# Kernel optimization log

Hardware: AMD Instinct MI355X
Metric: run time of the kernel (lower is better)

## Reference

```python
import jax, jax.numpy as jnp
import numpy as np

N_NODES = 50000
N_EDGES = 800000
D_IN = 64
D_OUT = 64
D_HID = 64
EPS = 1e-5


def _init_params(key):
    ks = jax.random.split(key, 12)
    s = 0.05
    p = {}
    p["W_lin"] = jax.random.normal(ks[0], (D_IN, D_OUT), jnp.float32) * s
    p["W_src"] = jax.random.normal(ks[1], (D_IN, D_OUT), jnp.float32) * s
    p["W_dst"] = jax.random.normal(ks[2], (D_IN, D_OUT), jnp.float32) * s
    p["pos_w1"] = jax.random.normal(ks[3], (3, D_HID), jnp.float32) * s
    p["pos_b1"] = jnp.zeros((D_HID,), jnp.float32)
    p["pos_w2"] = jax.random.normal(ks[4], (D_HID, D_OUT), jnp.float32) * s
    p["pos_b2"] = jnp.zeros((D_OUT,), jnp.float32)
    p["attn_w1"] = jax.random.normal(ks[5], (D_OUT, D_HID), jnp.float32) * s
    p["attn_b1"] = jnp.zeros((D_HID,), jnp.float32)
    p["attn_w2"] = jax.random.normal(ks[6], (D_HID, D_OUT), jnp.float32) * s
    p["attn_b2"] = jnp.zeros((D_OUT,), jnp.float32)
    p["gamma"] = jnp.ones((D_OUT,), jnp.float32)
    p["beta"] = jnp.zeros((D_OUT,), jnp.float32)
    return p


def setup_inputs() -> dict:
    key = jax.random.key(0)
    k1, k2, k3, k4 = jax.random.split(key, 4)
    inp = {
        "x": jax.random.normal(k1, (N_NODES, D_IN), jnp.float32),
        "pos": jax.random.normal(k2, (N_NODES, 3), jnp.float32),
        "edge_index": jax.random.randint(k3, (2, N_EDGES), 0, N_NODES, jnp.int64),
    }
    inp.update(_init_params(k4))
    return inp


def _segment_softmax(alpha, seg, num_segments):
    # channel-wise softmax over edges sharing the same destination node
    m = jax.ops.segment_max(alpha, seg, num_segments=num_segments)  # [N, D]
    e = jnp.exp(alpha - m[seg])
    z = jax.ops.segment_sum(e, seg, num_segments=num_segments)  # [N, D]
    return e / (z[seg] + 1e-16)


def reference(x, pos, edge_index, W_lin, W_src, W_dst,
              pos_w1, pos_b1, pos_w2, pos_b2,
              attn_w1, attn_b1, attn_w2, attn_b2, gamma, beta):
    N = x.shape[0]
    # add self loops (PointTransformerConv default add_self_loops=True)
    loops = jnp.arange(N, dtype=edge_index.dtype)
    src = jnp.concatenate([edge_index[0], loops])  # j
    dst = jnp.concatenate([edge_index[1], loops])  # i (aggregation target)

    x_val = x @ W_lin          # [N, D] value projection
    a_src = x @ W_src          # alpha_j source term
    a_dst = x @ W_dst          # alpha_i destination term

    # per-edge positional encoding: pos_nn(pos_i - pos_j), two Linears, no activation
    rel = pos[dst] - pos[src]                         # [E, 3]
    delta = (rel @ pos_w1 + pos_b1) @ pos_w2 + pos_b2  # [E, D]

    # attention logits: attn_nn(alpha_i - alpha_j + delta)
    alpha = a_dst[dst] - a_src[src] + delta
    alpha = (alpha @ attn_w1 + attn_b1) @ attn_w2 + attn_b2  # [E, D]
    alpha = _segment_softmax(alpha, dst, N)

    # message and scatter-sum aggregation
    msg = alpha * (x_val[src] + delta)                # [E, D]
    out = jax.ops.segment_sum(msg, dst, num_segments=N)  # [N, D]

    out = jax.nn.elu(out)

    # BatchNorm over nodes (training-mode batch stats, biased var, eps=1e-5)
    mean = jnp.mean(out, axis=0)
    var = jnp.var(out, axis=0)
    out = (out - mean) * jax.lax.rsqrt(var + EPS) * gamma + beta
    return out
```

## Files before the change

### kernel.cpp

```cpp
#include <hip/hip_runtime.h>
#include <cmath>


__device__ __forceinline__ unsigned bf16r(float f) {
    unsigned u = __float_as_uint(f);
    return (u + 0x7fffu + ((u >> 16) & 1u)) >> 16;
}
__device__ __forceinline__ float bfhi(unsigned u) { return __uint_as_float(u & 0xffff0000u); }
__device__ __forceinline__ float bflo(unsigned u) { return __uint_as_float(u << 16); }

__device__ __forceinline__ void gemm_tile(const float (*xs)[68], const float (*Wl)[64],
                                          int tx, int ty, float acc[4][4])
{
    #pragma unroll
    for (int i = 0; i < 4; ++i)
        #pragma unroll
        for (int j = 0; j < 4; ++j) acc[i][j] = 0.f;
    for (int k = 0; k < 64; k += 4) {
        float4 b0 = *(const float4*)&Wl[k + 0][4 * tx];
        float4 b1 = *(const float4*)&Wl[k + 1][4 * tx];
        float4 b2 = *(const float4*)&Wl[k + 2][4 * tx];
        float4 b3 = *(const float4*)&Wl[k + 3][4 * tx];
        #pragma unroll
        for (int i = 0; i < 4; ++i) {
            float4 a = *(const float4*)&xs[4 * ty + i][k];
            acc[i][0] += a.x * b0.x + a.y * b1.x + a.z * b2.x + a.w * b3.x;
            acc[i][1] += a.x * b0.y + a.y * b1.y + a.z * b2.y + a.w * b3.y;
            acc[i][2] += a.x * b0.z + a.y * b1.z + a.z * b2.z + a.w * b3.z;
            acc[i][3] += a.x * b0.w + a.y * b1.w + a.z * b2.w + a.w * b3.w;
        }
    }
}

__global__ __launch_bounds__(256) void k_pre1(
    const float* __restrict__ attn_w1, const float* __restrict__ attn_w2,
    const float* __restrict__ pos_w1, const float* __restrict__ pos_b1,
    const float* __restrict__ pos_w2, const float* __restrict__ pos_b2,
    float* __restrict__ A2, float* __restrict__ M3, float* __restrict__ bc,
    int* __restrict__ cnt, float* __restrict__ stats, int n_nodes)
{
    int t = threadIdx.x;
    if (blockIdx.x == 0) {
        __shared__ __align__(16) float As[64][68];
        __shared__ __align__(16) float Bs[64][64];
        int lk = t & 63, lr = t >> 6;
        for (int i = 0; i < 16; ++i) {
            As[lr + 4 * i][lk] = attn_w1[(lr + 4 * i) * 64 + lk];
            Bs[lr + 4 * i][lk] = attn_w2[(lr + 4 * i) * 64 + lk];
        }
        __syncthreads();
        int tx = t & 15, ty = t >> 4;
        float acc[4][4];
        gemm_tile(As, Bs, tx, ty, acc);
        #pragma unroll
        for (int i = 0; i < 4; ++i)
            *(float4*)&A2[(4 * ty + i) * 64 + 4 * tx] =
                make_float4(acc[i][0], acc[i][1], acc[i][2], acc[i][3]);
    } else if (blockIdx.x == 1) {
        int c = t & 63, q = t >> 6;
        if (q < 3) {
            float acc = 0.f;
            for (int h = 0; h < 64; ++h) acc += pos_w1[q * 64 + h] * pos_w2[h * 64 + c];
            M3[q * 64 + c] = acc;
        } else {
            float accb = 0.f;
            for (int h = 0; h < 64; ++h) accb += pos_b1[h] * pos_w2[h * 64 + c];
            bc[c] = accb + pos_b2[c];
        }
    } else {
        if (blockIdx.x == 2 && t < 128) stats[t] = 0.f;
        int idx = (blockIdx.x - 2) * 256 + t;
        int stride = (gridDim.x - 2) * 256;
        for (int i = idx; i < n_nodes; i += stride) cnt[i] = 0;
    }
}

__global__ __launch_bounds__(256) void k_pre2(
    const float* __restrict__ W_src, const float* __restrict__ A2,
    const float* __restrict__ M3,
    float* __restrict__ Wsrc2, float* __restrict__ M5)
{
    int t = threadIdx.x;
    if (blockIdx.x == 0) {
        __shared__ __align__(16) float As[64][68];
        __shared__ __align__(16) float Bs[64][64];
        int lk = t & 63, lr = t >> 6;
        for (int i = 0; i < 16; ++i) {
            As[lr + 4 * i][lk] = W_src[(lr + 4 * i) * 64 + lk];
            Bs[lr + 4 * i][lk] = A2[(lr + 4 * i) * 64 + lk];
        }
        __syncthreads();
        int tx = t & 15, ty = t >> 4;
        float acc[4][4];
        gemm_tile(As, Bs, tx, ty, acc);
        #pragma unroll
        for (int i = 0; i < 4; ++i)
            *(float4*)&Wsrc2[(4 * ty + i) * 64 + 4 * tx] =
                make_float4(acc[i][0], acc[i][1], acc[i][2], acc[i][3]);
    } else {
        int c = t & 63, q = t >> 6;
        if (q < 3) {
            float acc = 0.f;
            for (int k = 0; k < 64; ++k) acc += M3[q * 64 + k] * A2[k * 64 + c];
            M5[q * 64 + c] = acc;
        }
    }
}

__global__ __launch_bounds__(256, 4) void k_gemm_pair_hist(
    const float* __restrict__ x, const float* __restrict__ pos,
    const float* __restrict__ Wsrc2, const float* __restrict__ Wlin,
    const float* __restrict__ M3, const float* __restrict__ M5,
    unsigned* __restrict__ pairbf, int n_nodes,
    const int* __restrict__ ei, int* __restrict__ cnt, int n_edges, int G)
{
    int t = threadIdx.x;
    if ((int)blockIdx.x >= G) {
        int idx = ((int)blockIdx.x - G) * 256 + t;
        int stride = ((int)gridDim.x - G) * 256;
        for (int i = idx; i < n_edges; i += stride)
            atomicAdd(&cnt[ei[n_edges + i]], 1);
        return;
    }
    __shared__ __align__(16) float xs[64][68];
    __shared__ __align__(16) float Wl[64][64];
    __shared__ float ps[192];
    __shared__ float m3s[192], m5s[192];
    int tx = t & 15;
    int ty = t >> 4;
    int nbase = blockIdx.x * 64;
    int lk = t & 63;
    int lr = t >> 6;

    for (int i = 0; i < 16; ++i) {
        int n = lr + 4 * i;
        int gn = nbase + n;
        xs[n][lk] = (gn < n_nodes) ? x[gn * 64 + lk] : 0.f;
    }
    if (t < 192) {
        int gi = nbase * 3 + t;
        ps[t] = (gi < n_nodes * 3) ? pos[gi] : 0.f;
        m3s[t] = M3[t];
        m5s[t] = M5[t];
    }
    for (int i = 0; i < 16; ++i) Wl[lr + 4 * i][lk] = Wsrc2[(lr + 4 * i) * 64 + lk];
    __syncthreads();

    float acc_s[4][4];
    gemm_tile(xs, Wl, tx, ty, acc_s);

    __syncthreads();
    for (int i = 0; i < 16; ++i) Wl[lr + 4 * i][lk] = Wlin[(lr + 4 * i) * 64 + lk];
    __syncthreads();

    float acc_x[4][4];
    gemm_tile(xs, Wl, tx, ty, acc_x);

    #pragma unroll
    for (int i = 0; i < 4; ++i) {
        int n = 4 * ty + i;
        int gn = nbase + n;
        if (gn < n_nodes) {
            float px = ps[3 * n], py = ps[3 * n + 1], pz = ps[3 * n + 2];
            int c0 = 4 * tx;
            float g50 = px * m5s[c0]     + py * m5s[64 + c0]     + pz * m5s[128 + c0];
            float g51 = px * m5s[c0 + 1] + py * m5s[64 + c0 + 1] + pz * m5s[128 + c0 + 1];
            float g52 = px * m5s[c0 + 2] + py * m5s[64 + c0 + 2] + pz * m5s[128 + c0 + 2];
            float g53 = px * m5s[c0 + 3] + py * m5s[64 + c0 + 3] + pz * m5s[128 + c0 + 3];
            float g30 = px * m3s[c0]     + py * m3s[64 + c0]     + pz * m3s[128 + c0];
            float g31 = px * m3s[c0 + 1] + py * m3s[64 + c0 + 1] + pz * m3s[128 + c0 + 1];
            float g32 = px * m3s[c0 + 2] + py * m3s[64 + c0 + 2] + pz * m3s[128 + c0 + 2];
            float g33 = px * m3s[c0 + 3] + py * m3s[64 + c0 + 3] + pz * m3s[128 + c0 + 3];
            uint4 w;
            w.x = (bf16r(__expf(-(acc_s[i][0] + g50))) << 16) | bf16r(acc_x[i][0] - g30);
            w.y = (bf16r(__expf(-(acc_s[i][1] + g51))) << 16) | bf16r(acc_x[i][1] - g31);
            w.z = (bf16r(__expf(-(acc_s[i][2] + g52))) << 16) | bf16r(acc_x[i][2] - g32);
            w.w = (bf16r(__expf(-(acc_s[i][3] + g53))) << 16) | bf16r(acc_x[i][3] - g33);
            *(uint4*)&pairbf[gn * 64 + c0] = w;
        }
    }
}

#define SCAN_CHUNK 4096

__global__ __launch_bounds__(256) void k_scan_partial(const int* __restrict__ cnt,
                                                      int* __restrict__ bsum, int n)
{
    __shared__ int wsh[4];
    int b = blockIdx.x, t = threadIdx.x;
    int base = b * SCAN_CHUNK + t * 16;
    int s = 0;
    #pragma unroll
    for (int i = 0; i < 16; ++i) {
        int idx = base + i;
        if (idx < n) s += cnt[idx];
    }
    for (int off = 32; off; off >>= 1) s += __shfl_down(s, off, 64);
    int lane = t & 63, wv = t >> 6;
    if (lane == 0) wsh[wv] = s;
    __syncthreads();
    if (t == 0) bsum[b] = wsh[0] + wsh[1] + wsh[2] + wsh[3];
}

__global__ __launch_bounds__(256) void k_scan_final(const int* __restrict__ cnt,
                                                    const int* __restrict__ bsum,
                                                    int* __restrict__ rowptr,
                                                    int* __restrict__ cursor,
                                                    int n, int nch, int n_edges)
{
    __shared__ int wsh[4];
    __shared__ int bb;
    int b = blockIdx.x, t = threadIdx.x;
    if (t == 0) {
        int acc = 0;
        for (int c = 0; c < b; ++c) acc += bsum[c];
        bb = acc;
        if (b == nch - 1) rowptr[n] = n_edges;
    }
    int base = b * SCAN_CHUNK + t * 16;
    int v[16];
    int s = 0;
    #pragma unroll
    for (int i = 0; i < 16; ++i) {
        int idx = base + i;
        v[i] = (idx < n) ? cnt[idx] : 0;
        s += v[i];
    }
    int lane = t & 63, wv = t >> 6;
    int inc = s;
    for (int off = 1; off < 64; off <<= 1) {
        int u = __shfl_up(inc, off, 64);
        if (lane >= off) inc += u;
    }
    if (lane == 63) wsh[wv] = inc;
    __syncthreads();
    if (t == 0) {
        int acc = 0;
        for (int w = 0; w < 4; ++w) { int tmp = wsh[w]; wsh[w] = acc; acc += tmp; }
    }
    __syncthreads();
    int run = bb + wsh[wv] + inc - s;
    #pragma unroll
    for (int i = 0; i < 16; ++i) {
        int idx = base + i;
        if (idx < n) {
            rowptr[idx] = run;
            cursor[idx] = run;
            run += v[i];
        }
    }
}

__global__ __launch_bounds__(256) void k_scatter(const int* __restrict__ ei,
                                                 int* __restrict__ cursor,
                                                 int* __restrict__ csr_src,
                                                 int n_edges)
{
    int i = blockIdx.x * blockDim.x + threadIdx.x;
    if (i < n_edges) {
        int dst = ei[n_edges + i];
        int p = atomicAdd(&cursor[dst], 1);
        csr_src[p] = ei[i] * 64;
    }
}

__global__ __launch_bounds__(256) void k_gather(
    const int* __restrict__ rowptr, const int* __restrict__ csr_src,
    const unsigned* __restrict__ pairbf, const float* __restrict__ pos,
    const float* __restrict__ M3, const float* __restrict__ bc,
    float* __restrict__ out, float* __restrict__ stats, int n_nodes)
{
    int t = threadIdx.x;
    int c = t & 63;
    float bcc = bc[c];
    float m30 = M3[c], m31 = M3[64 + c], m32 = M3[128 + c];

    int wid = (blockIdx.x * blockDim.x + t) >> 6;
    int nw = (gridDim.x * blockDim.x) >> 6;

    float lsum = 0.f, lsq = 0.f;

    for (int i = wid; i < n_nodes; i += nw) {
        int beg = rowptr[i], end = rowptr[i + 1];
        float px = pos[3 * i], py = pos[3 * i + 1], pz = pos[3 * i + 2];
        float ddi = bcc + px * m30 + py * m31 + pz * m32;
        unsigned up = pairbf[i * 64 + c];
        float w = bfhi(up);
        float zz = w;
        float SS = w * bflo(up);

        int k = beg;
        for (; k + 8 <= end; k += 8) {
            int s0 = csr_src[k],     s1 = csr_src[k + 1];
            int s2 = csr_src[k + 2], s3 = csr_src[k + 3];
            int s4 = csr_src[k + 4], s5 = csr_src[k + 5];
            int s6 = csr_src[k + 6], s7 = csr_src[k + 7];
            unsigned u0 = pairbf[s0 + c], u1 = pairbf[s1 + c];
            unsigned u2 = pairbf[s2 + c], u3 = pairbf[s3 + c];
            unsigned u4 = pairbf[s4 + c], u5 = pairbf[s5 + c];
            unsigned u6 = pairbf[s6 + c], u7 = pairbf[s7 + c];
            float w0 = bfhi(u0), w1 = bfhi(u1), w2 = bfhi(u2), w3 = bfhi(u3);
            float w4 = bfhi(u4), w5 = bfhi(u5), w6 = bfhi(u6), w7 = bfhi(u7);
            zz += ((w0 + w1) + (w2 + w3)) + ((w4 + w5) + (w6 + w7));
            SS += w0 * bflo(u0) + w1 * bflo(u1) + w2 * bflo(u2) + w3 * bflo(u3)
                + w4 * bflo(u4) + w5 * bflo(u5) + w6 * bflo(u6) + w7 * bflo(u7);
        }
        for (; k < end; ++k) {
            unsigned u0 = pairbf[csr_src[k] + c];
            float w0 = bfhi(u0);
            zz += w0;
            SS += w0 * bflo(u0);
        }

        float v = SS / zz + ddi;
        v = (v > 0.f) ? v : expm1f(v);
        out[i * 64 + c] = v;
        lsum += v;
        lsq += v * v;
    }

    __shared__ float sred[256], sred2[256];
    sred[t] = lsum;
    sred2[t] = lsq;
    __syncthreads();
    if (t < 64) {
        float s = sred[t] + sred[t + 64] + sred[t + 128] + sred[t + 192];
        float q = sred2[t] + sred2[t + 64] + sred2[t + 128] + sred2[t + 192];
        unsafeAtomicAdd(&stats[t], s);
        unsafeAtomicAdd(&stats[64 + t], q);
    }
}

__global__ __launch_bounds__(256) void k_bn(
    float4* __restrict__ out4, const float* __restrict__ stats,
    const float* __restrict__ gamma, const float* __restrict__ beta,
    int total4, float inv_n)
{
    __shared__ float ssc[64], ssh[64];
    int t = threadIdx.x;
    if (t < 64) {
        float mean = stats[t] * inv_n;
        float var = stats[64 + t] * inv_n - mean * mean;
        float scale = (1.0f / sqrtf(var + 1e-5f)) * gamma[t];
        ssc[t] = scale;
        ssh[t] = beta[t] - mean * scale;
    }
    __syncthreads();
    for (int idx = blockIdx.x * blockDim.x + t; idx < total4;
         idx += gridDim.x * blockDim.x) {
        float4 v = out4[idx];
        int c0 = (idx << 2) & 63;
        v.x = v.x * ssc[c0]     + ssh[c0];
        v.y = v.y * ssc[c0 + 1] + ssh[c0 + 1];
        v.z = v.z * ssc[c0 + 2] + ssh[c0 + 2];
        v.w = v.w * ssc[c0 + 3] + ssh[c0 + 3];
        out4[idx] = v;
    }
}

extern "C" void kernel_launch(void* const* d_in, const int* in_sizes, int n_in,
                              void* d_out, int out_size, void* d_ws, size_t ws_size,
                              hipStream_t stream)
{
    const float* x        = (const float*)d_in[0];
    const float* pos      = (const float*)d_in[1];
    const int*   ei       = (const int*)d_in[2];
    const float* W_lin    = (const float*)d_in[3];
    const float* W_src    = (const float*)d_in[4];
    const float* pos_w1   = (const float*)d_in[6];
    const float* pos_b1   = (const float*)d_in[7];
    const float* pos_w2   = (const float*)d_in[8];
    const float* pos_b2   = (const float*)d_in[9];
    const float* attn_w1  = (const float*)d_in[10];
    const float* attn_w2  = (const float*)d_in[12];
    const float* gamma    = (const float*)d_in[14];
    const float* beta     = (const float*)d_in[15];

    int n_nodes = in_sizes[0] / 64;
    int n_edges = in_sizes[2] / 2;
    int total = n_nodes * 64;
    int nch = (n_nodes + SCAN_CHUNK - 1) / SCAN_CHUNK;

    unsigned* pairbf = (unsigned*)d_ws;
    float* A2    = (float*)(pairbf + total);
    float* Wsrc2 = A2 + 4096;
    float* M3    = Wsrc2 + 4096;
    float* M5    = M3 + 192;
    float* bc    = M5 + 192;
    float* stats = bc + 64;
    int*   cnt     = (int*)(stats + 128);
    int*   rowptr  = cnt + n_nodes;
    int*   cursor  = rowptr + n_nodes + 1;
    int*   csr_src = cursor + n_nodes;
    int*   bsum    = csr_src + n_edges;

    int G = (n_nodes + 63) / 64;

    k_pre1<<<18, 256, 0, stream>>>(attn_w1, attn_w2, pos_w1, pos_b1, pos_w2,
                                   pos_b2, A2, M3, bc, cnt, stats, n_nodes);
    k_pre2<<<2, 256, 0, stream>>>(W_src, A2, M3, Wsrc2, M5);
    k_gemm_pair_hist<<<G + 512, 256, 0, stream>>>(
        x, pos, Wsrc2, W_lin, M3, M5, pairbf, n_nodes, ei, cnt, n_edges, G);
    k_scan_partial<<<nch, 256, 0, stream>>>(cnt, bsum, n_nodes);
    k_scan_final<<<nch, 256, 0, stream>>>(cnt, bsum, rowptr, cursor,
                                          n_nodes, nch, n_edges);
    k_scatter<<<(n_edges + 255) / 256, 256, 0, stream>>>(ei, cursor, csr_src, n_edges);
    k_gather<<<2048, 256, 0, stream>>>(rowptr, csr_src, pairbf, pos, M3, bc,
                                       (float*)d_out, stats, n_nodes);
    k_bn<<<2048, 256, 0, stream>>>((float4*)d_out, stats, gamma, beta, total / 4,
                                   1.0f / (float)n_nodes);
}
```

Before: 203.6 us.

## Merge precompute kernels, vectorize histogram/scatter, split gather edges across half-waves

Folds the two small precompute kernels into one, computing Wsrc2 through shared memory and M5 through a chained small matmul, which removes a launch. The histogram and scatter kernels now read edge indices as int4, so each thread handles four edges. The gather kernel has each lane load two channels (uint2), and the two 32-lane halves of a wave take alternate 8-edge chunks, combined with a cross-half shuffle. The aim is more edges in flight per wave and fewer load instructions, at the cost of extra shuffles, half the lanes idling in the epilogue, and an alignment assumption for the int4 reads.

```diff
diff --git a/kernel.cpp b/kernel.cpp
--- a/kernel.cpp
+++ b/kernel.cpp
@@ -32,11 +32,13 @@
     }
 }
 
-__global__ __launch_bounds__(256) void k_pre1(
-    const float* __restrict__ attn_w1, const float* __restrict__ attn_w2,
+__global__ __launch_bounds__(256) void k_pre(
+    const float* __restrict__ W_src,
     const float* __restrict__ pos_w1, const float* __restrict__ pos_b1,
     const float* __restrict__ pos_w2, const float* __restrict__ pos_b2,
-    float* __restrict__ A2, float* __restrict__ M3, float* __restrict__ bc,
+    const float* __restrict__ attn_w1, const float* __restrict__ attn_w2,
+    float* __restrict__ Wsrc2, float* __restrict__ M3, float* __restrict__ M5,
+    float* __restrict__ bc,
     int* __restrict__ cnt, float* __restrict__ stats, int n_nodes)
 {
     int t = threadIdx.x;
@@ -52,58 +54,51 @@
         int tx = t & 15, ty = t >> 4;
         float acc[4][4];
         gemm_tile(As, Bs, tx, ty, acc);
+        __syncthreads();
         #pragma unroll
         for (int i = 0; i < 4; ++i)
-            *(float4*)&A2[(4 * ty + i) * 64 + 4 * tx] =
-                make_float4(acc[i][0], acc[i][1], acc[i][2], acc[i][3]);
+            #pragma unroll
+            for (int j = 0; j < 4; ++j)
+                Bs[4 * ty + i][4 * tx + j] = acc[i][j];
+        for (int i = 0; i < 16; ++i)
+            As[lr + 4 * i][lk] = W_src[(lr + 4 * i) * 64 + lk];
+        __syncthreads();
+        float acc2[4][4];
+        gemm_tile(As, Bs, tx, ty, acc2);
+        #pragma unroll
+        for (int i = 0; i < 4; ++i)
+            *(float4*)&Wsrc2[(4 * ty + i) * 64 + 4 * tx] =
+                make_float4(acc2[i][0], acc2[i][1], acc2[i][2], acc2[i][3]);
     } else if (blockIdx.x == 1) {
+        __shared__ float m3s[192], ts[192];
         int c = t & 63, q = t >> 6;
         if (q < 3) {
             float acc = 0.f;
             for (int h = 0; h < 64; ++h) acc += pos_w1[q * 64 + h] * pos_w2[h * 64 + c];
+            m3s[q * 64 + c] = acc;
             M3[q * 64 + c] = acc;
         } else {
             float accb = 0.f;
             for (int h = 0; h < 64; ++h) accb += pos_b1[h] * pos_w2[h * 64 + c];
             bc[c] = accb + pos_b2[c];
         }
+        __syncthreads();
+        if (q < 3) {
+            float acc = 0.f;
+            for (int k = 0; k < 64; ++k) acc += m3s[q * 64 + k] * attn_w1[k * 64 + c];
+            ts[q * 64 + c] = acc;
+        }
+        __syncthreads();
+        if (q < 3) {
+            float acc = 0.f;
+            for (int k = 0; k < 64; ++k) acc += ts[q * 64 + k] * attn_w2[k * 64 + c];
+            M5[q * 64 + c] = acc;
+        }
     } else {
         if (blockIdx.x == 2 && t < 128) stats[t] = 0.f;
         int idx = (blockIdx.x - 2) * 256 + t;
         int stride = (gridDim.x - 2) * 256;
         for (int i = idx; i < n_nodes; i += stride) cnt[i] = 0;
-    }
-}
-
-__global__ __launch_bounds__(256) void k_pre2(
-    const float* __restrict__ W_src, const float* __restrict__ A2,
-    const float* __restrict__ M3,
-    float* __restrict__ Wsrc2, float* __restrict__ M5)
-{
-    int t = threadIdx.x;
-    if (blockIdx.x == 0) {
-        __shared__ __align__(16) float As[64][68];
-        __shared__ __align__(16) float Bs[64][64];
-        int lk = t & 63, lr = t >> 6;
-        for (int i = 0; i < 16; ++i) {
-            As[lr + 4 * i][lk] = W_src[(lr + 4 * i) * 64 + lk];
-            Bs[lr + 4 * i][lk] = A2[(lr + 4 * i) * 64 + lk];
-        }
-        __syncthreads();
-        int tx = t & 15, ty = t >> 4;
-        float acc[4][4];
-        gemm_tile(As, Bs, tx, ty, acc);
-        #pragma unroll
-        for (int i = 0; i < 4; ++i)
-            *(float4*)&Wsrc2[(4 * ty + i) * 64 + 4 * tx] =
-                make_float4(acc[i][0], acc[i][1], acc[i][2], acc[i][3]);
-    } else {
-        int c = t & 63, q = t >> 6;
-        if (q < 3) {
-            float acc = 0.f;
-            for (int k = 0; k < 64; ++k) acc += M3[q * 64 + k] * A2[k * 64 + c];
-            M5[q * 64 + c] = acc;
-        }
     }
 }
 
@@ -118,7 +113,16 @@
     if ((int)blockIdx.x >= G) {
         int idx = ((int)blockIdx.x - G) * 256 + t;
         int stride = ((int)gridDim.x - G) * 256;
-        for (int i = idx; i < n_edges; i += stride)
+        int n4 = n_edges >> 2;
+        const int4* d4 = (const int4*)(ei + n_edges);
+        for (int i = idx; i < n4; i += stride) {
+            int4 d = d4[i];
+            atomicAdd(&cnt[d.x], 1);
+            atomicAdd(&cnt[d.y], 1);
+            atomicAdd(&cnt[d.z], 1);
+            atomicAdd(&cnt[d.w], 1);
+        }
+        for (int i = (n4 << 2) + idx; i < n_edges; i += stride)
             atomicAdd(&cnt[ei[n_edges + i]], 1);
         return;
     }
@@ -256,78 +260,116 @@
                                                  int* __restrict__ csr_src,
                                                  int n_edges)
 {
-    int i = blockIdx.x * blockDim.x + threadIdx.x;
-    if (i < n_edges) {
-        int dst = ei[n_edges + i];
-        int p = atomicAdd(&cursor[dst], 1);
-        csr_src[p] = ei[i] * 64;
+    int i4 = blockIdx.x * blockDim.x + threadIdx.x;
+    int n4 = n_edges >> 2;
+    if (i4 < n4) {
+        int4 sv = ((const int4*)ei)[i4];
+        int4 dv = ((const int4*)(ei + n_edges))[i4];
+        int p;
+        p = atomicAdd(&cursor[dv.x], 1); csr_src[p] = sv.x * 32;
+        p = atomicAdd(&cursor[dv.y], 1); csr_src[p] = sv.y * 32;
+        p = atomicAdd(&cursor[dv.z], 1); csr_src[p] = sv.z * 32;
+        p = atomicAdd(&cursor[dv.w], 1); csr_src[p] = sv.w * 32;
+    } else {
+        int e = (n4 << 2) + (i4 - n4);
+        if (e < n_edges) {
+            int dst = ei[n_edges + e];
+            int p = atomicAdd(&cursor[dst], 1);
+            csr_src[p] = ei[e] * 32;
+        }
     }
 }
 
 __global__ __launch_bounds__(256) void k_gather(
     const int* __restrict__ rowptr, const int* __restrict__ csr_src,
-    const unsigned* __restrict__ pairbf, const float* __restrict__ pos,
+    const uint2* __restrict__ pb2, const float* __restrict__ pos,
     const float* __restrict__ M3, const float* __restrict__ bc,
     float* __restrict__ out, float* __restrict__ stats, int n_nodes)
 {
     int t = threadIdx.x;
-    int c = t & 63;
-    float bcc = bc[c];
-    float m30 = M3[c], m31 = M3[64 + c], m32 = M3[128 + c];
+    int lane = t & 63;
+    int s = lane & 31;
+    int h = lane >> 5;
+    int c0 = 2 * s;
+    float bc0 = bc[c0], bc1 = bc[c0 + 1];
+    float m30a = M3[c0],     m31a = M3[64 + c0],     m32a = M3[128 + c0];
+    float m30b = M3[c0 + 1], m31b = M3[64 + c0 + 1], m32b = M3[128 + c0 + 1];
 
     int wid = (blockIdx.x * blockDim.x + t) >> 6;
     int nw = (gridDim.x * blockDim.x) >> 6;
 
-    float lsum = 0.f, lsq = 0.f;
+    float lsx = 0.f, lqx = 0.f, lsy = 0.f, lqy = 0.f;
 
     for (int i = wid; i < n_nodes; i += nw) {
         int beg = rowptr[i], end = rowptr[i + 1];
-        float px = pos[3 * i], py = pos[3 * i + 1], pz = pos[3 * i + 2];
-        float ddi = bcc + px * m30 + py * m31 + pz * m32;
-        unsigned up = pairbf[i * 64 + c];
-        float w = bfhi(up);
-        float zz = w;
-        float SS = w * bflo(up);
-
-        int k = beg;
-        for (; k + 8 <= end; k += 8) {
-            int s0 = csr_src[k],     s1 = csr_src[k + 1];
-            int s2 = csr_src[k + 2], s3 = csr_src[k + 3];
-            int s4 = csr_src[k + 4], s5 = csr_src[k + 5];
-            int s6 = csr_src[k + 6], s7 = csr_src[k + 7];
-            unsigned u0 = pairbf[s0 + c], u1 = pairbf[s1 + c];
-            unsigned u2 = pairbf[s2 + c], u3 = pairbf[s3 + c];
-            unsigned u4 = pairbf[s4 + c], u5 = pairbf[s5 + c];
-            unsigned u6 = pairbf[s6 + c], u7 = pairbf[s7 + c];
-            float w0 = bfhi(u0), w1 = bfhi(u1), w2 = bfhi(u2), w3 = bfhi(u3);
-            float w4 = bfhi(u4), w5 = bfhi(u5), w6 = bfhi(u6), w7 = bfhi(u7);
-            zz += ((w0 + w1) + (w2 + w3)) + ((w4 + w5) + (w6 + w7));
-            SS += w0 * bflo(u0) + w1 * bflo(u1) + w2 * bflo(u2) + w3 * bflo(u3)
-                + w4 * bflo(u4) + w5 * bflo(u5) + w6 * bflo(u6) + w7 * bflo(u7);
-        }
-        for (; k < end; ++k) {
-            unsigned u0 = pairbf[csr_src[k] + c];
-            float w0 = bfhi(u0);
-            zz += w0;
-            SS += w0 * bflo(u0);
-        }
-
-        float v = SS / zz + ddi;
-        v = (v > 0.f) ? v : expm1f(v);
-        out[i * 64 + c] = v;
-        lsum += v;
-        lsq += v * v;
-    }
-
-    __shared__ float sred[256], sred2[256];
-    sred[t] = lsum;
-    sred2[t] = lsq;
-    __syncthreads();
-    if (t < 64) {
-        float s = sred[t] + sred[t + 64] + sred[t + 128] + sred[t + 192];
-        float q = sred2[t] + sred2[t + 64] + sred2[t + 128] + sred2[t + 192];
-        unsafeAtomicAdd(&stats[t], s);
-        unsafeAtomicAdd(&stats[64 + t], q);
+        float zzx = 0.f, zzy = 0.f, SSx = 0.f, SSy = 0.f;
+        if (h == 0) {
+            uint2 up = pb2[i * 32 + s];
+            float w0 = bfhi(up.x), w1 = bfhi(up.y);
+            zzx = w0; SSx = w0 * bflo(up.x);
+            zzy = w1; SSy = w1 * bflo(up.y);
+        }
+        int k0 = beg;
+        for (; k0 + 16 <= end; k0 += 16) {
+            int kk = k0 + h * 8;
+            int e0 = csr_src[kk],     e1 = csr_src[kk + 1];
+            int e2 = csr_src[kk + 2], e3 = csr_src[kk + 3];
+            int e4 = csr_src[kk + 4], e5 = csr_src[kk + 5];
+            int e6 = csr_src[kk + 6], e7 = csr_src[kk + 7];
+            uint2 u0 = pb2[e0 + s], u1 = pb2[e1 + s];
+            uint2 u2 = pb2[e2 + s], u3 = pb2[e3 + s];
+            uint2 u4 = pb2[e4 + s], u5 = pb2[e5 + s];
+            uint2 u6 = pb2[e6 + s], u7 = pb2[e7 + s];
+            float a0 = bfhi(u0.x), a1 = bfhi(u1.x), a2 = bfhi(u2.x), a3 = bfhi(u3.x);
+            float a4 = bfhi(u4.x), a5 = bfhi(u5.x), a6 = bfhi(u6.x), a7 = bfhi(u7.x);
+            float b0 = bfhi(u0.y), b1 = bfhi(u1.y), b2 = bfhi(u2.y), b3 = bfhi(u3.y);
+            float b4 = bfhi(u4.y), b5 = bfhi(u5.y), b6 = bfhi(u6.y), b7 = bfhi(u7.y);
+            zzx += ((a0 + a1) + (a2 + a3)) + ((a4 + a5) + (a6 + a7));
+            zzy += ((b0 + b1) + (b2 + b3)) + ((b4 + b5) + (b6 + b7));
+            SSx += a0 * bflo(u0.x) + a1 * bflo(u1.x) + a2 * bflo(u2.x) + a3 * bflo(u3.x)
+                 + a4 * bflo(u4.x) + a5 * bflo(u5.x) + a6 * bflo(u6.x) + a7 * bflo(u7.x);
+            SSy += b0 * bflo(u0.y) + b1 * bflo(u1.y) + b2 * bflo(u2.y) + b3 * bflo(u3.y)
+                 + b4 * bflo(u4.y) + b5 * bflo(u5.y) + b6 * bflo(u6.y) + b7 * bflo(u7.y);
+        }
+        int r = end - k0;
+        int lo = h * 8;
+        int hi = min(r, 8 + lo);
+        for (int k = k0 + lo; k < k0 + hi; ++k) {
+            uint2 u = pb2[csr_src[k] + s];
+            float w0 = bfhi(u.x), w1 = bfhi(u.y);
+            zzx += w0; SSx += w0 * bflo(u.x);
+            zzy += w1; SSy += w1 * bflo(u.y);
+        }
+        zzx += __shfl_xor(zzx, 32, 64);
+        SSx += __shfl_xor(SSx, 32, 64);
+        zzy += __shfl_xor(zzy, 32, 64);
+        SSy += __shfl_xor(SSy, 32, 64);
+        if (h == 0) {
+            float px = pos[3 * i], py = pos[3 * i + 1], pz = pos[3 * i + 2];
+            float ddi0 = bc0 + px * m30a + py * m31a + pz * m32a;
+            float ddi1 = bc1 + px * m30b + py * m31b + pz * m32b;
+            float v0 = SSx / zzx + ddi0;
+            float v1 = SSy / zzy + ddi1;
+            v0 = (v0 > 0.f) ? v0 : expm1f(v0);
+            v1 = (v1 > 0.f) ? v1 : expm1f(v1);
+            *(float2*)&out[i * 64 + c0] = make_float2(v0, v1);
+            lsx += v0; lqx += v0 * v0;
+            lsy += v1; lqy += v1 * v1;
+        }
+    }
+
+    __shared__ float shx[256], shqx[256], shy[256], shqy[256];
+    shx[t] = lsx; shqx[t] = lqx; shy[t] = lsy; shqy[t] = lqy;
+    __syncthreads();
+    if (t < 32) {
+        float ax  = shx[t]  + shx[t + 64]  + shx[t + 128]  + shx[t + 192];
+        float aqx = shqx[t] + shqx[t + 64] + shqx[t + 128] + shqx[t + 192];
+        float ay  = shy[t]  + shy[t + 64]  + shy[t + 128]  + shy[t + 192];
+        float aqy = shqy[t] + shqy[t + 64] + shqy[t + 128] + shqy[t + 192];
+        unsafeAtomicAdd(&stats[2 * t], ax);
+        unsafeAtomicAdd(&stats[2 * t + 1], ay);
+        unsafeAtomicAdd(&stats[64 + 2 * t], aqx);
+        unsafeAtomicAdd(&stats[64 + 2 * t + 1], aqy);
     }
 }
 
@@ -382,8 +424,7 @@
     int nch = (n_nodes + SCAN_CHUNK - 1) / SCAN_CHUNK;
 
     unsigned* pairbf = (unsigned*)d_ws;
-    float* A2    = (float*)(pairbf + total);
-    float* Wsrc2 = A2 + 4096;
+    float* Wsrc2 = (float*)(pairbf + total);
     float* M3    = Wsrc2 + 4096;
     float* M5    = M3 + 192;
     float* bc    = M5 + 192;
@@ -395,18 +436,19 @@
     int*   bsum    = csr_src + n_edges;
 
     int G = (n_nodes + 63) / 64;
-
-    k_pre1<<<18, 256, 0, stream>>>(attn_w1, attn_w2, pos_w1, pos_b1, pos_w2,
-                                   pos_b2, A2, M3, bc, cnt, stats, n_nodes);
-    k_pre2<<<2, 256, 0, stream>>>(W_src, A2, M3, Wsrc2, M5);
-    k_gemm_pair_hist<<<G + 512, 256, 0, stream>>>(
+    int n4 = n_edges >> 2;
+
+    k_pre<<<18, 256, 0, stream>>>(W_src, pos_w1, pos_b1, pos_w2, pos_b2,
+                                  attn_w1, attn_w2, Wsrc2, M3, M5, bc,
+                                  cnt, stats, n_nodes);
+    k_gemm_pair_hist<<<G + 256, 256, 0, stream>>>(
         x, pos, Wsrc2, W_lin, M3, M5, pairbf, n_nodes, ei, cnt, n_edges, G);
     k_scan_partial<<<nch, 256, 0, stream>>>(cnt, bsum, n_nodes);
     k_scan_final<<<nch, 256, 0, stream>>>(cnt, bsum, rowptr, cursor,
                                           n_nodes, nch, n_edges);
-    k_scatter<<<(n_edges + 255) / 256, 256, 0, stream>>>(ei, cursor, csr_src, n_edges);
-    k_gather<<<2048, 256, 0, stream>>>(rowptr, csr_src, pairbf, pos, M3, bc,
-                                       (float*)d_out, stats, n_nodes);
+    k_scatter<<<(n4 + 4 + 255) / 256, 256, 0, stream>>>(ei, cursor, csr_src, n_edges);
+    k_gather<<<2048, 256, 0, stream>>>(rowptr, csr_src, (const uint2*)pairbf,
+                                       pos, M3, bc, (float*)d_out, stats, n_nodes);
     k_bn<<<2048, 256, 0, stream>>>((float4*)d_out, stats, gamma, beta, total / 4,
                                    1.0f / (float)n_nodes);
 }
```

After: 270.9 us. +33.1%, slower.
